# Performance work log

Hardware: AMD Instinct MI355X
Metric: run time of the kernel (lower is better)

The kernel has to match this reference:

```python
import jax, jax.numpy as jnp
import numpy as np

N_Q = 4; K = 4; IMG = 28; PAD = IMG + 2  # pad right/bottom so edge windows exist
N_WIN = 14 * 14  # stride-2 windows over 28x28


def _window_idx():
    # Faithful to torch: flatten the (possibly truncated) window row-major,
    # then pad with zeros AT THE END of the flattened vector.
    zero = PAD * PAD - 1  # padded image is zero there
    rows = []
    for i in range(0, IMG - 1, 2):
        for j in range(0, IMG - 1, 2):
            h = min(K, IMG - i); w = min(K, IMG - j)
            ids = [(i + r) * PAD + (j + c) for r in range(h) for c in range(w)]
            ids += [zero] * (K * K - len(ids))
            rows.append(ids)
    return np.asarray(rows, np.int32)  # [196, 16]

_WIDX = _window_idx()
# wire 0 is the most-significant bit of the 16-dim statevector index
_BITS = ((np.arange(16)[None, :] >> (3 - np.arange(4))[:, None]) & 1)
_ZSIGN = (1.0 - 2.0 * _BITS).astype(np.float32)  # [4, 16] PauliZ eigenvalues
# Four CRZ gates (control i, target (i+1)%4) are all diagonal -> combined diagonal phase
_CRZ_SIGNS = np.zeros(16, np.float32)
for _b in range(16):
    s = 0
    for _i in range(4):
        c = (_b >> (3 - _i)) & 1
        t = (_b >> (3 - ((_i + 1) % 4))) & 1
        s += c * (2 * t - 1)
    _CRZ_SIGNS[_b] = s
_H = (np.array([[1, 1], [1, -1]], np.complex64) / np.sqrt(2.0)).astype(np.complex64)


def _rz(a):  # a [B] -> [B,2,2]: diag(e^{-i a/2}, e^{+i a/2})
    em = jnp.exp(-0.5j * a); ep = jnp.exp(0.5j * a); z = jnp.zeros_like(em)
    return jnp.stack([jnp.stack([em, z], -1), jnp.stack([z, ep], -1)], -2)


def _ry(a):  # a [...] -> [...,2,2]
    c = jnp.cos(0.5 * a); s = jnp.sin(0.5 * a)
    return jnp.stack([jnp.stack([c, -s], -1), jnp.stack([s, c], -1)], -2).astype(jnp.complex64)


def _apply1q(state, U, w):  # state [B,16], U [B,2,2] or [2,2], wire w (0=MSB)
    L = 2 ** w; R = 2 ** (3 - w)
    s = state.reshape(-1, L, 2, R)
    if U.ndim == 2:
        out = jnp.einsum('ij,bajc->baic', U, s)
    else:
        out = jnp.einsum('bij,bajc->baic', U, s)
    return out.reshape(-1, 16)


def reference(x, crz_theta, ry_theta, fc1_w, fc1_b, fc2_w, fc2_b):
    B = x.shape[0]
    xp = jnp.pad(x[:, 0], ((0, 0), (0, 2), (0, 2))).reshape(B, -1)  # [B, 900]
    wins = xp[:, jnp.asarray(_WIDX)]              # [B, 196, 16]
    wins = jnp.transpose(wins, (1, 0, 2))         # [196, B, 16] for scan

    crz_diag = jnp.exp(0.5j * crz_theta * jnp.asarray(_CRZ_SIGNS))  # [16]
    Ry = _ry(ry_theta)                            # shared trainable RY, [2,2]
    H = jnp.asarray(_H)
    zsT = jnp.asarray(_ZSIGN).T                   # [16, 4]

    def step(state, f):  # state [B,16] complex64 persists ACROSS windows (no reset in source)
        for w in range(4):
            # compose H then the encoder rotations on this wire into one 2x2 per batch elem
            U = jnp.broadcast_to(H, (B, 2, 2))
            n = 5 if w < 3 else 1  # wire 3 only gets rz(f[15])
            for i in range(n):
                a = f[:, w * 5 + i]
                M = _rz(a) if i % 2 == 0 else _ry(a)  # gates = rz,ry,rz,ry,rz
                U = jnp.einsum('bij,bjk->bik', M, U)
            state = _apply1q(state, U, w)
        state = state * crz_diag[None, :]          # ring of CRZ gates (diagonal)
        for w in range(4):
            state = _apply1q(state, Ry, w)
        probs = state.real ** 2 + state.imag ** 2
        return state, probs @ zsT                  # [B, 4] PauliZ expectations

    state0 = jnp.zeros((B, 16), jnp.complex64).at[:, 0].set(1.0)
    _, outs = jax.lax.scan(step, state0, wins)     # [196, B, 4]
    feats = jnp.transpose(outs, (1, 0, 2)).reshape(B, N_WIN * 4)  # window-major concat
    h1 = feats @ fc1_w.T + fc1_b
    h1 = jnp.where(h1 > 0, h1, 0.1 * h1)           # LeakyReLU(0.1)
    return h1 @ fc2_w.T + fc2_b


def setup_inputs() -> dict:
    key = jax.random.key(0)
    ks = jax.random.split(key, 7)
    B = 16384
    return {
        'x': jax.random.normal(ks[0], (B, 1, 28, 28), jnp.float32),
        'crz_theta': jax.random.normal(ks[1], (), jnp.float32),
        'ry_theta': jax.random.normal(ks[2], (), jnp.float32),
        'fc1_w': jax.random.normal(ks[3], (20, 784), jnp.float32) * 0.03,
        'fc1_b': jnp.zeros((20,), jnp.float32),
        'fc2_w': jax.random.normal(ks[4], (2, 20), jnp.float32) * 0.1,
        'fc2_b': jnp.zeros((2,), jnp.float32),
    }
```

## Files before the change

kernel.cpp:

```cpp
#include <hip/hip_runtime.h>

#define RS2f 0.70710678118654752f

#define QP_XOR1 0xB1
#define QP_XOR2 0x4E
#define QP_BC0  0x00
#define QP_BC1  0x55
#define QP_BC2  0xAA
#define QP_BC3  0xFF

typedef float v2f __attribute__((ext_vector_type(2)));

template<int CTRL> __device__ __forceinline__ float dppf(float x) {
  return __int_as_float(__builtin_amdgcn_update_dpp(
      0, __float_as_int(x), CTRL, 0xF, 0xF, true));
}
template<int CTRL> __device__ __forceinline__ v2f dpp2(v2f v) {
  v2f r; r.x = dppf<CTRL>(v.x); r.y = dppf<CTRL>(v.y); return r;
}

__device__ __forceinline__ float sxor(float x, int sm) {
  return __int_as_float(__float_as_int(x) ^ sm);
}
__device__ __forceinline__ v2f vsplat(float a) { v2f r; r.x = a; r.y = a; return r; }
__device__ __forceinline__ v2f vperp(v2f v) { v2f r; r.x = -v.y; r.y = v.x; return r; }
__device__ __forceinline__ v2f vperc(v2f v) { v2f r; r.x = v.y; r.y = -v.x; return r; }
__device__ __forceinline__ v2f vfma2(float a, v2f b, v2f c) {
  return __builtin_elementwise_fma(vsplat(a), b, c);
}
__device__ __forceinline__ v2f vmul2(float a, v2f b) { return vsplat(a) * b; }

__device__ __forceinline__ void build_gate(float a0, float a1, float a2, float a3, float a4,
                                           float &w0r, float &w0i, float &w1r, float &w1i) {
  float sBp, cBp, sBm, cBm, sC, cC, sP, cP, sM, cM;
  __sincosf(0.5f * (a1 + a3), &sBp, &cBp);
  __sincosf(0.5f * (a1 - a3), &sBm, &cBm);
  __sincosf(0.5f * a2,        &sC,  &cC);
  __sincosf(0.5f * (a0 + a4), &sP,  &cP);
  __sincosf(0.5f * (a0 - a4), &sM,  &cM);
  float m00r =  cBp * cC, m00i = -cBm * sC;
  float m01r = -sBp * cC, m01i =  sBm * sC;
  float alr = fmaf(m00r, cP,  m00i * sP);
  float ali = fmaf(m00i, cP, -m00r * sP);
  float ber = fmaf(m01r, cM, -m01i * sM);
  float bei = fmaf(m01i, cM,  m01r * sM);
  w0r = RS2f * (alr + ber); w0i = RS2f * (ali + bei);
  w1r = RS2f * (alr - ber); w1i = RS2f * (ali - bei);
}

#define PICK_FULL                                                            \
  a0 = l0 ? P[0][0] : l1 ? P[1][1] : l2 ? P[2][2] : P[3][3];                 \
  a1 = l0 ? P[0][1] : l1 ? P[1][2] : l2 ? P[2][3] : 0.f;                     \
  a2 = l0 ? P[0][2] : l1 ? P[1][3] : l2 ? P[3][0] : 0.f;                     \
  a3 = l0 ? P[0][3] : l1 ? P[2][0] : l2 ? P[3][1] : 0.f;                     \
  a4 = l0 ? P[1][0] : l1 ? P[2][1] : l2 ? P[3][2] : 0.f;

#define PICK_W2                                                              \
  a0 = l0 ? P[0][0] : l1 ? P[2][1] : 0.f;                                    \
  a1 = l0 ? P[0][1] : l1 ? P[3][0] : 0.f;                                    \
  a2 = l0 ? P[1][0] : l1 ? P[3][1] : 0.f;                                    \
  a3 = l0 ? P[1][1] : 0.f;                                                   \
  a4 = l0 ? P[2][0] : 0.f;

#define PICK_H2                                                              \
  a0 = l0 ? P[0][0] : l1 ? P[1][1] : 0.f;                                    \
  a1 = l0 ? P[0][1] : l1 ? P[1][2] : 0.f;                                    \
  a2 = l0 ? P[0][2] : l1 ? P[1][3] : 0.f;                                    \
  a3 = l0 ? P[0][3] : 0.f;                                                   \
  a4 = l0 ? P[1][0] : 0.f;

#define PICK_22                                                              \
  a0 = l0 ? P[0][0] : 0.f;                                                   \
  a1 = l0 ? P[0][1] : 0.f;                                                   \
  a2 = l0 ? P[1][0] : 0.f;                                                   \
  a3 = l0 ? P[1][1] : 0.f;                                                   \
  a4 = 0.f;

#define APPLY_Z do {                                                         \
  { float w0r = dppf<QP_BC0>(Wc0), w0i = dppf<QP_BC0>(Wc1);                  \
    float w1r = dppf<QP_BC0>(Wc2), w1i = dppf<QP_BC0>(Wc3);                  \
    float uar = sxor(w0r, sm0), uai = w0i;                                   \
    float ubr = w1r,            ubi = sxor(w1i, sm0);                        \
    _Pragma("unroll")                                                        \
    for (int k = 0; k < 4; ++k) {                                            \
      v2f p = dpp2<QP_XOR2>(s[k]);                                           \
      v2f a = s[k];                                                          \
      s[k] = vfma2(uar, a, vfma2(uai, vperp(a),                              \
                   vfma2(ubr, p, vmul2(ubi, vperp(p)))));                    \
    } }                                                                      \
  { float w0r = dppf<QP_BC1>(Wc0), w0i = dppf<QP_BC1>(Wc1);                  \
    float w1r = dppf<QP_BC1>(Wc2), w1i = dppf<QP_BC1>(Wc3);                  \
    float uar = sxor(w0r, sm1), uai = w0i;                                   \
    float ubr = w1r,            ubi = sxor(w1i, sm1);                        \
    _Pragma("unroll")                                                        \
    for (int k = 0; k < 4; ++k) {                                            \
      v2f p = dpp2<QP_XOR1>(s[k]);                                           \
      v2f a = s[k];                                                          \
      s[k] = vfma2(uar, a, vfma2(uai, vperp(a),                              \
                   vfma2(ubr, p, vmul2(ubi, vperp(p)))));                    \
    } }                                                                      \
  { float w0r = dppf<QP_BC2>(Wc0), w0i = dppf<QP_BC2>(Wc1);                  \
    float w1r = dppf<QP_BC2>(Wc2), w1i = dppf<QP_BC2>(Wc3);                  \
    float nw0r = -w0r, nw0i = -w0i;                                          \
    _Pragma("unroll")                                                        \
    for (int k = 0; k < 2; ++k) {                                            \
      v2f lo = s[k], hi = s[k+2];                                            \
      s[k]   = vfma2(w0r, lo, vfma2(w0i, vperp(lo),                          \
                     vfma2(w1r, hi, vmul2(w1i, vperp(hi)))));                \
      s[k+2] = vfma2(w1r, lo, vfma2(w1i, vperc(lo),                          \
                     vfma2(nw0r, hi, vmul2(nw0i, vperc(hi)))));              \
    } }                                                                      \
  { float w0r = dppf<QP_BC3>(Wc0), w0i = dppf<QP_BC3>(Wc1);                  \
    float w1r = dppf<QP_BC3>(Wc2), w1i = dppf<QP_BC3>(Wc3);                  \
    float nw0r = -w0r, nw0i = -w0i;                                          \
    _Pragma("unroll")                                                        \
    for (int k = 0; k < 4; k += 2) {                                         \
      v2f lo = s[k], hi = s[k+1];                                            \
      s[k]   = vfma2(w0r, lo, vfma2(w0i, vperp(lo),                          \
                     vfma2(w1r, hi, vmul2(w1i, vperp(hi)))));                \
      s[k+1] = vfma2(w1r, lo, vfma2(w1i, vperc(lo),                          \
                     vfma2(nw0r, hi, vmul2(nw0i, vperc(hi)))));              \
    } }                                                                      \
  _Pragma("unroll")                                                          \
  for (int k = 0; k < 4; ++k)                                                \
    s[k] = vfma2(czk[k], s[k], vmul2(szk[k], vperp(s[k])));                  \
  _Pragma("unroll")                                                          \
  for (int k = 0; k < 4; ++k) {                                              \
    v2f p = dpp2<QP_XOR2>(s[k]);                                             \
    s[k] = vfma2(cry, s[k], vmul2(sgn0, p));                                 \
  }                                                                          \
  _Pragma("unroll")                                                          \
  for (int k = 0; k < 4; ++k) {                                              \
    v2f p = dpp2<QP_XOR1>(s[k]);                                             \
    s[k] = vfma2(cry, s[k], vmul2(sgn1, p));                                 \
  }                                                                          \
  _Pragma("unroll")                                                          \
  for (int k = 0; k < 2; ++k) {                                              \
    v2f lo = s[k], hi = s[k+2];                                              \
    s[k]   = vfma2(cry, lo, vmul2(nsry, hi));                                \
    s[k+2] = vfma2(sry, lo, vmul2(cry, hi));                                 \
  }                                                                          \
  _Pragma("unroll")                                                          \
  for (int k = 0; k < 4; k += 2) {                                           \
    v2f lo = s[k], hi = s[k+1];                                              \
    s[k]   = vfma2(cry, lo, vmul2(nsry, hi));                                \
    s[k+1] = vfma2(sry, lo, vmul2(cry, hi));                                 \
  }                                                                          \
  { v2f q0 = s[0]*s[0], q1 = s[1]*s[1], q2 = s[2]*s[2], q3 = s[3]*s[3];      \
    float p0 = q0.x + q0.y, p1 = q1.x + q1.y;                                \
    float p2 = q2.x + q2.y, p3 = q3.x + q3.y;                                \
    float s01 = p0 + p1, s23 = p2 + p3;                                      \
    float t_  = s01 + s23;                                                   \
    np0 = sxor(t_, sm0);                                                     \
    np1 = sxor(t_, sm1);                                                     \
    np2 = s01 - s23;                                                         \
    np3 = (p0 - p1) + (p2 - p3);                                             \
  }                                                                          \
} while (0)

#define BF_FOLD do {                                                         \
  float o0 = pd0, o1 = pd1, o2 = pd2, o3 = pd3;                              \
  o0 += dppf<QP_XOR1>(o0); o0 += dppf<QP_XOR2>(o0);                          \
  o1 += dppf<QP_XOR1>(o1); o1 += dppf<QP_XOR2>(o1);                          \
  o2 += dppf<QP_XOR1>(o2); o2 += dppf<QP_XOR2>(o2);                          \
  o3 += dppf<QP_XOR1>(o3); o3 += dppf<QP_XOR2>(o3);                          \
  const float* wp = swl + pdWin * 4;                                         \
  float4 wv0 = *(const float4*)(wp);                                         \
  float4 wv1 = *(const float4*)(wp + 784);                                   \
  float4 wv2 = *(const float4*)(wp + 1568);                                  \
  float4 wv3 = *(const float4*)(wp + 2352);                                  \
  float4 wv4 = *(const float4*)(wp + 3136);                                  \
  h1[0] = fmaf(wv0.x, o0, fmaf(wv0.y, o1, fmaf(wv0.z, o2, fmaf(wv0.w, o3, h1[0])))); \
  h1[1] = fmaf(wv1.x, o0, fmaf(wv1.y, o1, fmaf(wv1.z, o2, fmaf(wv1.w, o3, h1[1])))); \
  h1[2] = fmaf(wv2.x, o0, fmaf(wv2.y, o1, fmaf(wv2.z, o2, fmaf(wv2.w, o3, h1[2])))); \
  h1[3] = fmaf(wv3.x, o0, fmaf(wv3.y, o1, fmaf(wv3.z, o2, fmaf(wv3.w, o3, h1[3])))); \
  h1[4] = fmaf(wv4.x, o0, fmaf(wv4.y, o1, fmaf(wv4.z, o2, fmaf(wv4.w, o3, h1[4])))); \
} while (0)

#define SHIFT_PEND(WIN)  pd0 = np0; pd1 = np1; pd2 = np2; pd3 = np3; pdWin = (WIN);
#define ROTATE_W  Wc0 = Wn0; Wc1 = Wn1; Wc2 = Wn2; Wc3 = Wn3;

__global__ void __launch_bounds__(256)
quanv_kernel(const float* __restrict__ x,
             const float* __restrict__ crz_t,
             const float* __restrict__ ry_t,
             const float* __restrict__ fc1_w,
             const float* __restrict__ fc1_b,
             const float* __restrict__ fc2_w,
             const float* __restrict__ fc2_b,
             float* __restrict__ out, int B)
{
  __shared__ float sw[20 * 784];
  const int tid = threadIdx.x;
  for (int i = tid; i < (20 * 784) / 4; i += 256)
    ((float4*)sw)[i] = ((const float4*)fc1_w)[i];
  __syncthreads();

  const int l = tid & 3;
  const int b = (blockIdx.x * 256 + tid) >> 2;
  if (b >= B) return;
  const float* img = x + (size_t)b * 784;
  const bool l0 = (l == 0), l1 = (l == 1), l2 = (l == 2);

  const float theta = crz_t[0];
  const float ryt   = ry_t[0];
  float cry, sry;
  __sincosf(0.5f * ryt, &sry, &cry);
  const float nsry = -sry;
  const float sgn0 = (l & 2) ? sry : -sry;
  const float sgn1 = (l & 1) ? sry : -sry;
  const int sm0 = (l & 2) ? (int)0x80000000 : 0;
  const int sm1 = (l & 1) ? (int)0x80000000 : 0;

  float g0,g1,g2,g3;
  if      (l == 0) { g0= 0.f; g1=-1.f; g2=-1.f; g3=0.f; }
  else if (l == 1) { g0=-1.f; g1=-2.f; g2= 0.f; g3=1.f; }
  else if (l == 2) { g0=-1.f; g1= 0.f; g2=-2.f; g3=1.f; }
  else             { g0= 0.f; g1= 1.f; g2= 1.f; g3=4.f; }
  float czk[4], szk[4];
  __sincosf(0.5f*theta*g0, &szk[0], &czk[0]);
  __sincosf(0.5f*theta*g1, &szk[1], &czk[1]);
  __sincosf(0.5f*theta*g2, &szk[2], &czk[2]);
  __sincosf(0.5f*theta*g3, &szk[3], &czk[3]);

  v2f s[4];
#pragma unroll
  for (int k = 0; k < 4; ++k) { s[k].x = 0.f; s[k].y = 0.f; }
  if (l == 0) s[0].x = 1.f;

  float h1[5];
#pragma unroll
  for (int j = 0; j < 5; ++j) h1[j] = 0.f;
  const float* swl = sw + 5 * l * 784;

  float P[4][4];
  float a0, a1, a2, a3, a4;
  float Wc0, Wc1, Wc2, Wc3, Wn0, Wn1, Wn2, Wn3;
  float np0, np1, np2, np3;
  float pd0 = 0.f, pd1 = 0.f, pd2 = 0.f, pd3 = 0.f;
  int pdWin = 0;

#pragma unroll 1
  for (int wi = 0; wi < 13; ++wi) {
    const float* imgw = img + (2 * wi) * 28;

#pragma unroll
    for (int r = 0; r < 4; ++r) {
      float4 v = *(const float4*)(imgw + r * 28);
      P[r][0]=v.x; P[r][1]=v.y; P[r][2]=v.z; P[r][3]=v.w;
    }
    PICK_FULL;
    build_gate(a0, a1, a2, a3, a4, Wc0, Wc1, Wc2, Wc3);

    float2 Q0 = *(const float2*)(imgw + 0 * 28 + 4);
    float2 Q1 = *(const float2*)(imgw + 1 * 28 + 4);
    float2 Q2 = *(const float2*)(imgw + 2 * 28 + 4);
    float2 Q3 = *(const float2*)(imgw + 3 * 28 + 4);

#pragma unroll 4
    for (int wj = 1; wj <= 12; ++wj) {
      P[0][0]=P[0][2]; P[0][1]=P[0][3]; P[0][2]=Q0.x; P[0][3]=Q0.y;
      P[1][0]=P[1][2]; P[1][1]=P[1][3]; P[1][2]=Q1.x; P[1][3]=Q1.y;
      P[2][0]=P[2][2]; P[2][1]=P[2][3]; P[2][2]=Q2.x; P[2][3]=Q2.y;
      P[3][0]=P[3][2]; P[3][1]=P[3][3]; P[3][2]=Q3.x; P[3][3]=Q3.y;
      const int c0n = (wj < 12) ? (2 * wj + 4) : 24;
      Q0 = *(const float2*)(imgw + 0 * 28 + c0n);
      Q1 = *(const float2*)(imgw + 1 * 28 + c0n);
      Q2 = *(const float2*)(imgw + 2 * 28 + c0n);
      Q3 = *(const float2*)(imgw + 3 * 28 + c0n);
      PICK_FULL;
      build_gate(a0, a1, a2, a3, a4, Wn0, Wn1, Wn2, Wn3);
      APPLY_Z;
      BF_FOLD;
      SHIFT_PEND(wi * 14 + wj - 1);
      ROTATE_W;
    }

#pragma unroll
    for (int r = 0; r < 4; ++r) {
      P[r][0] = P[r][2]; P[r][1] = P[r][3]; P[r][2] = 0.f; P[r][3] = 0.f;
    }
    PICK_W2;
    build_gate(a0, a1, a2, a3, a4, Wn0, Wn1, Wn2, Wn3);
    APPLY_Z;
    BF_FOLD;
    SHIFT_PEND(wi * 14 + 12);
    ROTATE_W;
    APPLY_Z;
    BF_FOLD;
    SHIFT_PEND(wi * 14 + 13);
  }

  {
    const float* imgw = img + 26 * 28;
#pragma unroll
    for (int r = 0; r < 2; ++r) {
      float4 v = *(const float4*)(imgw + r * 28);
      P[r][0]=v.x; P[r][1]=v.y; P[r][2]=v.z; P[r][3]=v.w;
    }
#pragma unroll
    for (int r = 2; r < 4; ++r) { P[r][0]=0.f; P[r][1]=0.f; P[r][2]=0.f; P[r][3]=0.f; }
    PICK_H2;
    build_gate(a0, a1, a2, a3, a4, Wc0, Wc1, Wc2, Wc3);

    float2 Q0 = *(const float2*)(imgw + 4);
    float2 Q1 = *(const float2*)(imgw + 28 + 4);

#pragma unroll 4
    for (int wj = 1; wj <= 12; ++wj) {
      P[0][0]=P[0][2]; P[0][1]=P[0][3]; P[0][2]=Q0.x; P[0][3]=Q0.y;
      P[1][0]=P[1][2]; P[1][1]=P[1][3]; P[1][2]=Q1.x; P[1][3]=Q1.y;
      const int c0n = (wj < 12) ? (2 * wj + 4) : 24;
      Q0 = *(const float2*)(imgw + c0n);
      Q1 = *(const float2*)(imgw + 28 + c0n);
      PICK_H2;
      build_gate(a0, a1, a2, a3, a4, Wn0, Wn1, Wn2, Wn3);
      APPLY_Z;
      BF_FOLD;
      SHIFT_PEND(182 + wj - 1);
      ROTATE_W;
    }

    P[0][0]=P[0][2]; P[0][1]=P[0][3]; P[0][2]=0.f; P[0][3]=0.f;
    P[1][0]=P[1][2]; P[1][1]=P[1][3]; P[1][2]=0.f; P[1][3]=0.f;
    PICK_22;
    build_gate(a0, a1, a2, a3, a4, Wn0, Wn1, Wn2, Wn3);
    APPLY_Z;
    BF_FOLD;
    SHIFT_PEND(182 + 12);
    ROTATE_W;
    APPLY_Z;
    BF_FOLD;
    SHIFT_PEND(182 + 13);
  }

  BF_FOLD;

  float pa = 0.f, pb = 0.f;
#pragma unroll
  for (int j = 0; j < 5; ++j) {
    const int r = 5 * l + j;
    float v = h1[j] + fc1_b[r];
    v = (v > 0.f) ? v : 0.1f * v;
    pa = fmaf(fc2_w[r],      v, pa);
    pb = fmaf(fc2_w[20 + r], v, pb);
  }
  pa += dppf<QP_XOR1>(pa); pa += dppf<QP_XOR2>(pa);
  pb += dppf<QP_XOR1>(pb); pb += dppf<QP_XOR2>(pb);
  if (l == 0) {
    float2 res; res.x = pa + fc2_b[0]; res.y = pb + fc2_b[1];
    *(float2*)(out + (size_t)b * 2) = res;
  }
}

extern "C" void kernel_launch(void* const* d_in, const int* in_sizes, int n_in,
                              void* d_out, int out_size, void* d_ws, size_t ws_size,
                              hipStream_t stream) {
  const float* x      = (const float*)d_in[0];
  const float* crz_t  = (const float*)d_in[1];
  const float* ry_t   = (const float*)d_in[2];
  const float* fc1_w  = (const float*)d_in[3];
  const float* fc1_b  = (const float*)d_in[4];
  const float* fc2_w  = (const float*)d_in[5];
  const float* fc2_b  = (const float*)d_in[6];
  float* out = (float*)d_out;
  const int B = in_sizes[0] / 784;
  const int grid = (B * 4 + 255) / 256;
  quanv_kernel<<<grid, 256, 0, stream>>>(x, crz_t, ry_t, fc1_w, fc1_b,
                                         fc2_w, fc2_b, out, B);
}
```

Before: 224.0 us.

## Fold trailing Ry layer into next encoding gate and measure analytically

Removes the per-window explicit Ry rotation layer, which used DPP cross-lane shuffles and butterfly FMAs on the statevector. Its effect on the next window is absorbed into the first Hadamard-like combination of that window's encoding gate through modified u/v coefficients. The PauliZ expectations of the rotated state are computed directly from cross terms of the unrotated state using cos/sin of theta. This cuts shuffle and FMA work per window, but adds cross-product reductions and new gate coefficients whose correctness at the row boundaries (wi==0 versus later rows) has to hold.

```diff
diff --git a/kernel.cpp b/kernel.cpp
--- a/kernel.cpp
+++ b/kernel.cpp
@@ -28,9 +28,13 @@
 __device__ __forceinline__ v2f vfma2(float a, v2f b, v2f c) {
   return __builtin_elementwise_fma(vsplat(a), b, c);
 }
+__device__ __forceinline__ v2f vfma2v(v2f a, v2f b, v2f c) {
+  return __builtin_elementwise_fma(a, b, c);
+}
 __device__ __forceinline__ v2f vmul2(float a, v2f b) { return vsplat(a) * b; }
 
 __device__ __forceinline__ void build_gate(float a0, float a1, float a2, float a3, float a4,
+                                           float u, float v,
                                            float &w0r, float &w0i, float &w1r, float &w1i) {
   float sBp, cBp, sBm, cBm, sC, cC, sP, cP, sM, cM;
   __sincosf(0.5f * (a1 + a3), &sBp, &cBp);
@@ -44,8 +48,8 @@
   float ali = fmaf(m00i, cP, -m00r * sP);
   float ber = fmaf(m01r, cM, -m01i * sM);
   float bei = fmaf(m01i, cM,  m01r * sM);
-  w0r = RS2f * (alr + ber); w0i = RS2f * (ali + bei);
-  w1r = RS2f * (alr - ber); w1i = RS2f * (ali - bei);
+  w0r = fmaf(u, alr, v * ber); w0i = fmaf(u, ali, v * bei);
+  w1r = fmaf(v, alr, -u * ber); w1i = fmaf(v, ali, -u * bei);
 }
 
 #define PICK_FULL                                                            \
@@ -124,37 +128,28 @@
   _Pragma("unroll")                                                          \
   for (int k = 0; k < 4; ++k)                                                \
     s[k] = vfma2(czk[k], s[k], vmul2(szk[k], vperp(s[k])));                  \
-  _Pragma("unroll")                                                          \
-  for (int k = 0; k < 4; ++k) {                                              \
-    v2f p = dpp2<QP_XOR2>(s[k]);                                             \
-    s[k] = vfma2(cry, s[k], vmul2(sgn0, p));                                 \
-  }                                                                          \
-  _Pragma("unroll")                                                          \
-  for (int k = 0; k < 4; ++k) {                                              \
-    v2f p = dpp2<QP_XOR1>(s[k]);                                             \
-    s[k] = vfma2(cry, s[k], vmul2(sgn1, p));                                 \
-  }                                                                          \
-  _Pragma("unroll")                                                          \
-  for (int k = 0; k < 2; ++k) {                                              \
-    v2f lo = s[k], hi = s[k+2];                                              \
-    s[k]   = vfma2(cry, lo, vmul2(nsry, hi));                                \
-    s[k+2] = vfma2(sry, lo, vmul2(cry, hi));                                 \
-  }                                                                          \
-  _Pragma("unroll")                                                          \
-  for (int k = 0; k < 4; k += 2) {                                           \
-    v2f lo = s[k], hi = s[k+1];                                              \
-    s[k]   = vfma2(cry, lo, vmul2(nsry, hi));                                \
-    s[k+1] = vfma2(sry, lo, vmul2(cry, hi));                                 \
-  }                                                                          \
+           \
   { v2f q0 = s[0]*s[0], q1 = s[1]*s[1], q2 = s[2]*s[2], q3 = s[3]*s[3];      \
     float p0 = q0.x + q0.y, p1 = q1.x + q1.y;                                \
     float p2 = q2.x + q2.y, p3 = q3.x + q3.y;                                \
     float s01 = p0 + p1, s23 = p2 + p3;                                      \
     float t_  = s01 + s23;                                                   \
-    np0 = sxor(t_, sm0);                                                     \
-    np1 = sxor(t_, sm1);                                                     \
-    np2 = s01 - s23;                                                         \
-    np3 = (p0 - p1) + (p2 - p3);                                             \
+    v2f xa0 = s[0] * dpp2<QP_XOR2>(s[0]);                                    \
+    xa0 = vfma2v(s[1], dpp2<QP_XOR2>(s[1]), xa0);                            \
+    xa0 = vfma2v(s[2], dpp2<QP_XOR2>(s[2]), xa0);                            \
+    xa0 = vfma2v(s[3], dpp2<QP_XOR2>(s[3]), xa0);                            \
+    v2f xa1 = s[0] * dpp2<QP_XOR1>(s[0]);                                    \
+    xa1 = vfma2v(s[1], dpp2<QP_XOR1>(s[1]), xa1);                            \
+    xa1 = vfma2v(s[2], dpp2<QP_XOR1>(s[2]), xa1);                            \
+    xa1 = vfma2v(s[3], dpp2<QP_XOR1>(s[3]), xa1);                            \
+    v2f xa2 = s[0] * s[2];  xa2 = vfma2v(s[1], s[3], xa2);                   \
+    v2f xa3 = s[0] * s[1];  xa3 = vfma2v(s[2], s[3], xa3);                   \
+    float x0 = xa0.x + xa0.y, x1 = xa1.x + xa1.y;                            \
+    float x2 = xa2.x + xa2.y, x3 = xa3.x + xa3.y;                            \
+    np0 = fmaf(ct, sxor(t_, sm0), -st  * x0);                                \
+    np1 = fmaf(ct, sxor(t_, sm1), -st  * x1);                                \
+    np2 = fmaf(ct, s01 - s23,     -st2 * x2);                                \
+    np3 = fmaf(ct, (p0 - p1) + (p2 - p3), -st2 * x3);                        \
   }                                                                          \
 } while (0)
 
@@ -206,9 +201,11 @@
   const float ryt   = ry_t[0];
   float cry, sry;
   __sincosf(0.5f * ryt, &sry, &cry);
-  const float nsry = -sry;
-  const float sgn0 = (l & 2) ? sry : -sry;
-  const float sgn1 = (l & 1) ? sry : -sry;
+  const float uH = RS2f * (cry + sry);
+  const float vH = RS2f * (cry - sry);
+  float st, ct;
+  __sincosf(ryt, &st, &ct);
+  const float st2 = 2.0f * st;
   const int sm0 = (l & 2) ? (int)0x80000000 : 0;
   const int sm1 = (l & 1) ? (int)0x80000000 : 0;
 
@@ -243,6 +240,8 @@
 #pragma unroll 1
   for (int wi = 0; wi < 13; ++wi) {
     const float* imgw = img + (2 * wi) * 28;
+    const float ug = (wi == 0) ? RS2f : uH;
+    const float vg = (wi == 0) ? RS2f : vH;
 
 #pragma unroll
     for (int r = 0; r < 4; ++r) {
@@ -250,7 +249,7 @@
       P[r][0]=v.x; P[r][1]=v.y; P[r][2]=v.z; P[r][3]=v.w;
     }
     PICK_FULL;
-    build_gate(a0, a1, a2, a3, a4, Wc0, Wc1, Wc2, Wc3);
+    build_gate(a0, a1, a2, a3, a4, ug, vg, Wc0, Wc1, Wc2, Wc3);
 
     float2 Q0 = *(const float2*)(imgw + 0 * 28 + 4);
     float2 Q1 = *(const float2*)(imgw + 1 * 28 + 4);
@@ -269,7 +268,7 @@
       Q2 = *(const float2*)(imgw + 2 * 28 + c0n);
       Q3 = *(const float2*)(imgw + 3 * 28 + c0n);
       PICK_FULL;
-      build_gate(a0, a1, a2, a3, a4, Wn0, Wn1, Wn2, Wn3);
+      build_gate(a0, a1, a2, a3, a4, uH, vH, Wn0, Wn1, Wn2, Wn3);
       APPLY_Z;
       BF_FOLD;
       SHIFT_PEND(wi * 14 + wj - 1);
@@ -281,7 +280,7 @@
       P[r][0] = P[r][2]; P[r][1] = P[r][3]; P[r][2] = 0.f; P[r][3] = 0.f;
     }
     PICK_W2;
-    build_gate(a0, a1, a2, a3, a4, Wn0, Wn1, Wn2, Wn3);
+    build_gate(a0, a1, a2, a3, a4, uH, vH, Wn0, Wn1, Wn2, Wn3);
     APPLY_Z;
     BF_FOLD;
     SHIFT_PEND(wi * 14 + 12);
@@ -301,7 +300,7 @@
 #pragma unroll
     for (int r = 2; r < 4; ++r) { P[r][0]=0.f; P[r][1]=0.f; P[r][2]=0.f; P[r][3]=0.f; }
     PICK_H2;
-    build_gate(a0, a1, a2, a3, a4, Wc0, Wc1, Wc2, Wc3);
+    build_gate(a0, a1, a2, a3, a4, uH, vH, Wc0, Wc1, Wc2, Wc3);
 
     float2 Q0 = *(const float2*)(imgw + 4);
     float2 Q1 = *(const float2*)(imgw + 28 + 4);
@@ -314,7 +313,7 @@
       Q0 = *(const float2*)(imgw + c0n);
       Q1 = *(const float2*)(imgw + 28 + c0n);
       PICK_H2;
-      build_gate(a0, a1, a2, a3, a4, Wn0, Wn1, Wn2, Wn3);
+      build_gate(a0, a1, a2, a3, a4, uH, vH, Wn0, Wn1, Wn2, Wn3);
       APPLY_Z;
       BF_FOLD;
       SHIFT_PEND(182 + wj - 1);
@@ -324,7 +323,7 @@
     P[0][0]=P[0][2]; P[0][1]=P[0][3]; P[0][2]=0.f; P[0][3]=0.f;
     P[1][0]=P[1][2]; P[1][1]=P[1][3]; P[1][2]=0.f; P[1][3]=0.f;
     PICK_22;
-    build_gate(a0, a1, a2, a3, a4, Wn0, Wn1, Wn2, Wn3);
+    build_gate(a0, a1, a2, a3, a4, uH, vH, Wn0, Wn1, Wn2, Wn3);
     APPLY_Z;
     BF_FOLD;
     SHIFT_PEND(182 + 12);
```

New measurement: 223.5 us. About the same (-0.2%).
